# Performance work log

Hardware: AMD Instinct MI355X
Metric: run time of the kernel (lower is better)

The kernel has to match this reference:

```python
import jax, jax.numpy as jnp
import numpy as np

S, B, IN, HID, H, D, DFF, L, NC, EMB = 1024, 32, 3072, 256, 16, 16, 1024, 4, 1623, 10


def setup_inputs() -> dict:
    key = jax.random.key(0)
    ks = jax.random.split(key, 12)
    w = lambda k, shp: 0.02 * jax.random.normal(k, shp, dtype=jnp.float32)
    return {
        "x": jax.random.normal(ks[0], (S, B, IN), dtype=jnp.float32),
        "fb": jax.random.randint(ks[1], (S, B), 0, NC),
        "fc1_w": w(ks[2], (HID, IN)),
        "fc1_b": jnp.zeros((HID,), jnp.float32),
        "emb": w(ks[3], (NC, EMB)),
        "proj_w": w(ks[4], (HID, HID + EMB)),
        "proj_b": jnp.zeros((HID,), jnp.float32),
        "ln1_g": jnp.ones((L, HID), jnp.float32),
        "ln1_b": jnp.zeros((L, HID), jnp.float32),
        "slow_w": w(ks[5], (L, H * (3 * D + 1), HID)),
        "out_w": w(ks[6], (L, HID, H * D)),
        "ln2_g": jnp.ones((L, HID), jnp.float32),
        "ln2_b": jnp.zeros((L, HID), jnp.float32),
        "ff1_w": w(ks[7], (L, DFF, HID)),
        "ff1_b": jnp.zeros((L, DFF), jnp.float32),
        "ff2_w": w(ks[8], (L, HID, DFF)),
        "ff2_b": jnp.zeros((L, HID), jnp.float32),
        "outl_w": w(ks[9], (NC, HID)),
        "outl_b": jnp.zeros((NC,), jnp.float32),
    }


def _ln(x, g, b):
    m = jnp.mean(x, -1, keepdims=True)
    v = jnp.mean(jnp.square(x - m), -1, keepdims=True)
    return (x - m) * jax.lax.rsqrt(v + 1e-5) * g + b


def _delta_attn(x, g, b, sw, ow):
    # x: (S, B, HID); delta-rule fast-weight linear attention
    s, bsz, _ = x.shape
    qkvb = jnp.einsum('sbi,oi->sbo', _ln(x, g, b), sw).reshape(s, bsz, H, 3 * D + 1)
    q, k, v, beta = jnp.split(qkvb, [D, 2 * D, 3 * D], axis=-1)
    q = jax.nn.softmax(q, axis=-1)      # sum-normalized feature map
    k = jax.nn.softmax(k, axis=-1)
    beta = jax.nn.sigmoid(beta)         # (S,B,H,1)

    def step(W, inp):
        qt, kt, vt, bt = inp            # (B,H,D),(B,H,D),(B,H,D),(B,H,1)
        v_old = jnp.einsum('bhkv,bhk->bhv', W, kt)
        v_new = bt * vt + (1.0 - bt) * v_old
        W = W + jnp.einsum('bhk,bhv->bhkv', kt, v_new - v_old)
        return W, jnp.einsum('bhkv,bhk->bhv', W, qt)

    W0 = jnp.zeros((bsz, H, D, D), x.dtype)
    _, o = jax.lax.scan(step, W0, (q, k, v, beta))   # o: (S,B,H,D)
    return x + jnp.einsum('sbi,oi->sbo', o.reshape(s, bsz, H * D), ow)


def _ffn(x, g, b, w1, b1, w2, b2):
    h = jax.nn.relu(jnp.einsum('sbi,oi->sbo', _ln(x, g, b), w1) + b1)
    return x + jnp.einsum('sbi,oi->sbo', h, w2) + b2


def reference(x, fb, fc1_w, fc1_b, emb, proj_w, proj_b, ln1_g, ln1_b, slow_w,
              out_w, ln2_g, ln2_b, ff1_w, ff1_b, ff2_w, ff2_b, outl_w, outl_b):
    h = jnp.einsum('sbi,oi->sbo', x, fc1_w) + fc1_b
    h = jnp.concatenate([h, emb[fb]], axis=-1)
    h = jnp.einsum('sbi,oi->sbo', h, proj_w) + proj_b
    for l in range(L):
        h = _delta_attn(h, ln1_g[l], ln1_b[l], slow_w[l], out_w[l])
        h = _ffn(h, ln2_g[l], ln2_b[l], ff1_w[l], ff1_b[l], ff2_w[l], ff2_b[l])
    return jnp.einsum('sbi,oi->sbo', h, outl_w) + outl_b
```

## Files before the change

### kernel.cpp

```cpp
#include <hip/hip_runtime.h>
#include <hip/hip_bf16.h>

#define S_LEN  1024
#define B_SZ   32
#define IN_DIM 3072
#define HID    256
#define NHEAD  16
#define HDIM   16
#define DFF    1024
#define NLAYER 4
#define NCLS   1623
#define EMB_D  10
#define MROWS  (S_LEN * B_SZ)
#define QROW   56

using bf16   = __hip_bfloat16;
using short8 = __attribute__((ext_vector_type(8))) short;
using f32x4  = __attribute__((ext_vector_type(4))) float;

#define GLOAD16(g, l) __builtin_amdgcn_global_load_lds(                        \
    (const __attribute__((address_space(1))) void*)(g),                        \
    (__attribute__((address_space(3))) void*)(l), 16, 0, 0)

__device__ __forceinline__ float b2f(short s) {
    union { float f; unsigned u; } x;
    x.u = ((unsigned)(unsigned short)s) << 16;
    return x.f;
}

template<int FLAGS>
__global__ __launch_bounds__(256) void mgemm(
    const bf16* __restrict__ A, const bf16* __restrict__ W,
    const float* __restrict__ bias, void* C, int N, int K, int Wld)
{
    __shared__ bf16 sA[2][128 * 32];
    __shared__ bf16 sB[2][128 * 32];
    const int t    = threadIdx.x;
    const int lane = t & 63;
    const int wid  = t >> 6;
    const int wr   = wid >> 1, wc = wid & 1;
    const long bm  = (long)blockIdx.x * 128;
    const int  bn  = blockIdx.y * 128;
    const int  fr  = lane & 15;
    const int  fg  = lane >> 4;
    const int  row0 = t >> 2;
    const int  kq0  = (t & 3) << 3;

    f32x4 acc[4][4];
#pragma unroll
    for (int m = 0; m < 4; ++m)
#pragma unroll
        for (int n = 0; n < 4; ++n)
#pragma unroll
            for (int r = 0; r < 4; ++r) acc[m][n][r] = 0.f;

    const int nkt = K >> 5;

    auto stage = [&](int buf, int kt) {
        const int k0 = kt << 5;
        GLOAD16(A + (bm + row0)      * (long)K   + k0 + kq0, &sA[buf][(t      ) * 8]);
        GLOAD16(A + (bm + row0 + 64) * (long)K   + k0 + kq0, &sA[buf][(t + 256) * 8]);
        GLOAD16(W + (long)(bn + row0)      * Wld + k0 + kq0, &sB[buf][(t      ) * 8]);
        GLOAD16(W + (long)(bn + row0 + 64) * Wld + k0 + kq0, &sB[buf][(t + 256) * 8]);
    };

    stage(0, 0);
    __syncthreads();
    for (int kt = 0; kt < nkt; ++kt) {
        const int cur = kt & 1;
        if (kt + 1 < nkt) stage(cur ^ 1, kt + 1);
        short8 af[4], bg[4];
#pragma unroll
        for (int m = 0; m < 4; ++m)
            af[m] = *(const short8*)&sA[cur][(wr * 64 + m * 16 + fr) * 32 + fg * 8];
#pragma unroll
        for (int n = 0; n < 4; ++n)
            bg[n] = *(const short8*)&sB[cur][(wc * 64 + n * 16 + fr) * 32 + fg * 8];
#pragma unroll
        for (int m = 0; m < 4; ++m)
#pragma unroll
            for (int n = 0; n < 4; ++n)
                acc[m][n] = __builtin_amdgcn_mfma_f32_16x16x32_bf16(
                    af[m], bg[n], acc[m][n], 0, 0, 0);
        __syncthreads();
    }

    float bs[4];
#pragma unroll
    for (int n = 0; n < 4; ++n) {
        const int c = bn + wc * 64 + n * 16 + fr;
        bs[n] = ((FLAGS & 1) && c < N) ? bias[c] : 0.f;
    }
#pragma unroll
    for (int m = 0; m < 4; ++m) {
#pragma unroll
        for (int n = 0; n < 4; ++n) {
            const int c = bn + wc * 64 + n * 16 + fr;
            if (c < N) {
#pragma unroll
                for (int r = 0; r < 4; ++r) {
                    const long rw = bm + wr * 64 + m * 16 + fg * 4 + r;
                    float v = acc[m][n][r] + bs[n];
                    if (FLAGS & 2) v = fmaxf(v, 0.f);
                    if (FLAGS & 16) {
                        const int s = (int)(rw >> 5), b = (int)(rw & 31);
                        const int hh = c / 49, cc = c - hh * 49;
                        if (cc == 48) v = 1.f / (1.f + __expf(-v));
                        ((bf16*)C)[((long)(b * 16 + hh) * 1024 + s) * QROW + cc] =
                            __float2bfloat16(v);
                    } else if (FLAGS & 8) {
                        ((bf16*)C)[rw * N + c] = __float2bfloat16(v);
                    } else {
                        ((float*)C)[rw * N + c] = v;
                    }
                }
            }
        }
    }
}

template<int FLAGS>
__global__ __launch_bounds__(256) void gemm_ln(
    const bf16* __restrict__ A, const bf16* __restrict__ W,
    const float* __restrict__ bias, const float* __restrict__ lg,
    const float* __restrict__ lb, float* H, bf16* __restrict__ Y, int K)
{
    __shared__ bf16 sA[2][64 * 32];
    __shared__ bf16 sB[2][256 * 32];
    __shared__ float rsum[64][4];
    __shared__ float rsq[64][4];
    const int t    = threadIdx.x;
    const int lane = t & 63;
    const int w    = t >> 6;
    const int fr   = lane & 15;
    const int fg   = lane >> 4;
    const long bm  = (long)blockIdx.x * 64;

    f32x4 acc[4][4];
#pragma unroll
    for (int m = 0; m < 4; ++m)
#pragma unroll
        for (int n = 0; n < 4; ++n)
#pragma unroll
            for (int r = 0; r < 4; ++r) acc[m][n][r] = 0.f;

    const int nkt = K >> 5;
    auto stage = [&](int buf, int kt) {
        const int k0 = kt << 5;
        GLOAD16(A + (bm + (t >> 2)) * (long)K + k0 + ((t & 3) << 3),
                &sA[buf][t * 8]);
#pragma unroll
        for (int i = 0; i < 4; ++i)
            GLOAD16(W + (long)((i << 6) + (t >> 2)) * K + k0 + ((t & 3) << 3),
                    &sB[buf][(i * 256 + t) * 8]);
    };

    stage(0, 0);
    __syncthreads();
    for (int kt = 0; kt < nkt; ++kt) {
        const int cur = kt & 1;
        if (kt + 1 < nkt) stage(cur ^ 1, kt + 1);
        short8 af[4], bg[4];
#pragma unroll
        for (int m = 0; m < 4; ++m)
            af[m] = *(const short8*)&sA[cur][(m * 16 + fr) * 32 + fg * 8];
#pragma unroll
        for (int n = 0; n < 4; ++n)
            bg[n] = *(const short8*)&sB[cur][(w * 64 + n * 16 + fr) * 32 + fg * 8];
#pragma unroll
        for (int m = 0; m < 4; ++m)
#pragma unroll
            for (int n = 0; n < 4; ++n)
                acc[m][n] = __builtin_amdgcn_mfma_f32_16x16x32_bf16(
                    af[m], bg[n], acc[m][n], 0, 0, 0);
        __syncthreads();
    }

    float bs[4];
#pragma unroll
    for (int n = 0; n < 4; ++n) {
        const int c = w * 64 + n * 16 + fr;
        bs[n] = (FLAGS & 1) ? bias[c] : 0.f;
    }
    float ps[4][4], pq[4][4];
#pragma unroll
    for (int m = 0; m < 4; ++m)
#pragma unroll
        for (int r = 0; r < 4; ++r) { ps[m][r] = 0.f; pq[m][r] = 0.f; }
#pragma unroll
    for (int m = 0; m < 4; ++m)
#pragma unroll
        for (int n = 0; n < 4; ++n)
#pragma unroll
            for (int r = 0; r < 4; ++r) {
                const long rw = bm + m * 16 + fg * 4 + r;
                const int c = w * 64 + n * 16 + fr;
                float v = acc[m][n][r] + bs[n];
                if (FLAGS & 4) v += H[rw * HID + c];
                H[rw * HID + c] = v;
                acc[m][n][r] = v;
                ps[m][r] += v;
                pq[m][r] += v * v;
            }
    if (FLAGS & 8) {
#pragma unroll
        for (int m = 0; m < 4; ++m)
#pragma unroll
            for (int n = 0; n < 4; ++n)
#pragma unroll
                for (int r = 0; r < 4; ++r) {
                    const long rw = bm + m * 16 + fg * 4 + r;
                    const int c = w * 64 + n * 16 + fr;
                    Y[rw * HID + c] = __float2bfloat16(acc[m][n][r]);
                }
    } else {
#pragma unroll
        for (int m = 0; m < 4; ++m)
#pragma unroll
            for (int r = 0; r < 4; ++r) {
                float s = ps[m][r], q = pq[m][r];
                s += __shfl_xor(s, 1); q += __shfl_xor(q, 1);
                s += __shfl_xor(s, 2); q += __shfl_xor(q, 2);
                s += __shfl_xor(s, 4); q += __shfl_xor(q, 4);
                s += __shfl_xor(s, 8); q += __shfl_xor(q, 8);
                ps[m][r] = s; pq[m][r] = q;
            }
        if (fr == 0) {
#pragma unroll
            for (int m = 0; m < 4; ++m)
#pragma unroll
                for (int r = 0; r < 4; ++r) {
                    const int row = m * 16 + fg * 4 + r;
                    rsum[row][w] = ps[m][r];
                    rsq[row][w]  = pq[m][r];
                }
        }
        __syncthreads();
#pragma unroll
        for (int m = 0; m < 4; ++m)
#pragma unroll
            for (int r = 0; r < 4; ++r) {
                const int row = m * 16 + fg * 4 + r;
                const float4 s4 = *(const float4*)&rsum[row][0];
                const float4 q4 = *(const float4*)&rsq[row][0];
                const float S = (s4.x + s4.y) + (s4.z + s4.w);
                const float Q = (q4.x + q4.y) + (q4.z + q4.w);
                const float mean = S * (1.f / 256.f);
                const float inv  = rsqrtf(Q * (1.f / 256.f) - mean * mean + 1e-5f);
                const long rw = bm + row;
#pragma unroll
                for (int n = 0; n < 4; ++n) {
                    const int c = w * 64 + n * 16 + fr;
                    const float y = (acc[m][n][r] - mean) * inv * lg[c] + lb[c];
                    Y[rw * HID + c] = __float2bfloat16(y);
                }
            }
    }
}

__global__ __launch_bounds__(256) void fc1_k(
    const float* __restrict__ A, const bf16* __restrict__ W,
    const float* __restrict__ bias, bf16* __restrict__ hcat)
{
    __shared__ bf16 sA[2][128 * 32];
    __shared__ bf16 sB[2][128 * 32];
    const int t    = threadIdx.x;
    const int lane = t & 63;
    const int wid  = t >> 6;
    const int wr   = wid >> 1, wc = wid & 1;
    const long bm  = (long)blockIdx.x * 128;
    const int  bn  = blockIdx.y * 128;
    const int  fr  = lane & 15;
    const int  fg  = lane >> 4;
    const int  row0 = t >> 2;
    const int  kq0  = (t & 3) << 3;
    const int  arow = t >> 3;
    const int  ac4  = (t & 7) << 2;

    f32x4 acc[4][4];
#pragma unroll
    for (int m = 0; m < 4; ++m)
#pragma unroll
        for (int n = 0; n < 4; ++n)
#pragma unroll
            for (int r = 0; r < 4; ++r) acc[m][n][r] = 0.f;

    auto stageB = [&](int buf, int kt) {
        const int k0 = kt << 5;
        GLOAD16(W + (long)(bn + row0)      * IN_DIM + k0 + kq0, &sB[buf][(t      ) * 8]);
        GLOAD16(W + (long)(bn + row0 + 64) * IN_DIM + k0 + kq0, &sB[buf][(t + 256) * 8]);
    };
    float4 va[4];
    auto loadA = [&](int kt) {
        const int k0 = kt << 5;
#pragma unroll
        for (int rep = 0; rep < 4; ++rep)
            va[rep] = *(const float4*)(A + (bm + arow + rep * 32) * (long)IN_DIM + k0 + ac4);
    };
    auto writeA = [&](int buf) {
#pragma unroll
        for (int rep = 0; rep < 4; ++rep) {
            alignas(8) bf16 tb[4];
            tb[0] = __float2bfloat16(va[rep].x);
            tb[1] = __float2bfloat16(va[rep].y);
            tb[2] = __float2bfloat16(va[rep].z);
            tb[3] = __float2bfloat16(va[rep].w);
            *(ushort4*)&sA[buf][(arow + rep * 32) * 32 + ac4] = *(const ushort4*)tb;
        }
    };

    loadA(0);
    stageB(0, 0);
    writeA(0);
    __syncthreads();
    const int nkt = IN_DIM >> 5;
    for (int kt = 0; kt < nkt; ++kt) {
        const int cur = kt & 1;
        if (kt + 1 < nkt) { stageB(cur ^ 1, kt + 1); loadA(kt + 1); }
        short8 af[4], bg[4];
#pragma unroll
        for (int m = 0; m < 4; ++m)
            af[m] = *(const short8*)&sA[cur][(wr * 64 + m * 16 + fr) * 32 + fg * 8];
#pragma unroll
        for (int n = 0; n < 4; ++n)
            bg[n] = *(const short8*)&sB[cur][(wc * 64 + n * 16 + fr) * 32 + fg * 8];
#pragma unroll
        for (int m = 0; m < 4; ++m)
#pragma unroll
            for (int n = 0; n < 4; ++n)
                acc[m][n] = __builtin_amdgcn_mfma_f32_16x16x32_bf16(
                    af[m], bg[n], acc[m][n], 0, 0, 0);
        if (kt + 1 < nkt) writeA(cur ^ 1);
        __syncthreads();
    }

#pragma unroll
    for (int n = 0; n < 4; ++n) {
        const int c = bn + wc * 64 + n * 16 + fr;
        const float bsn = bias[c];
#pragma unroll
        for (int m = 0; m < 4; ++m)
#pragma unroll
            for (int r = 0; r < 4; ++r) {
                const long rw = bm + wr * 64 + m * 16 + fg * 4 + r;
                hcat[rw * 288 + c] = __float2bfloat16(acc[m][n][r] + bsn);
            }
    }
}

__global__ __launch_bounds__(256) void fillemb(
    const float* __restrict__ emb, const int* __restrict__ fb,
    bf16* __restrict__ hcat)
{
    const long row = (long)blockIdx.x * 8 + (threadIdx.x >> 5);
    const int c = threadIdx.x & 31;
    bf16 v = (c < EMB_D) ? __float2bfloat16(emb[(long)fb[row] * EMB_D + c])
                         : __float2bfloat16(0.f);
    hcat[row * 288 + 256 + c] = v;
}

__global__ __launch_bounds__(256) void cvtall(
    const float* __restrict__ fc1_w, const float* __restrict__ proj_w,
    const float* __restrict__ slow_w, const float* __restrict__ out_w,
    const float* __restrict__ ff1_w, const float* __restrict__ ff2_w,
    const float* __restrict__ outl_w, bf16* __restrict__ dst)
{
    for (long i = (long)blockIdx.x * 256 + threadIdx.x; i < 4562944L;
         i += (long)gridDim.x * 256) {
        float v;
        if (i < 786432L) {
            v = fc1_w[i];
        } else if (i < 860160L) {
            const long j = i - 786432L;
            const int r = (int)(j / 288), c = (int)(j - (long)r * 288);
            v = (c < 266) ? proj_w[(long)r * 266 + c] : 0.f;
        } else if (i < 1777664L) {
            const long j = i - 860160L;
            const int l = (int)(j / 229376);
            const long m = j - (long)l * 229376;
            const int r = (int)(m >> 8), c = (int)(m & 255);
            v = (r < 784) ? slow_w[(long)l * 200704 + (long)r * 256 + c] : 0.f;
        } else if (i < 2039808L) {
            v = out_w[i - 1777664L];
        } else if (i < 3088384L) {
            v = ff1_w[i - 2039808L];
        } else if (i < 4136960L) {
            v = ff2_w[i - 3088384L];
        } else {
            const long j = i - 4136960L;
            const int r = (int)(j >> 8), c = (int)(j & 255);
            v = (r < 1623) ? outl_w[(long)r * 256 + c] : 0.f;
        }
        dst[i] = __float2bfloat16(v);
    }
}

#define DOT16(dst, kr, s0, s1, s2, s3) do {                                    \
    float _pa = fmaf(kr[3],  (s0).w, fmaf(kr[2],  (s0).z, fmaf(kr[1],  (s0).y, kr[0]  * (s0).x))); \
    float _pb = fmaf(kr[7],  (s1).w, fmaf(kr[6],  (s1).z, fmaf(kr[5],  (s1).y, kr[4]  * (s1).x))); \
    float _pc = fmaf(kr[11], (s2).w, fmaf(kr[10], (s2).z, fmaf(kr[9],  (s2).y, kr[8]  * (s2).x))); \
    float _pd = fmaf(kr[15], (s3).w, fmaf(kr[14], (s3).z, fmaf(kr[13], (s3).y, kr[12] * (s3).x))); \
    dst = (_pa + _pb) + (_pc + _pd);                                           \
} while (0)

__global__ __launch_bounds__(256) void coef_k(
    const bf16* __restrict__ qkvb, float* __restrict__ cfb)
{
    __shared__ float wrkc[4][16 * 52];
    __shared__ float Gm[4][16 * 17];
    __shared__ float Mql[4][16 * 17];
    const int tid = threadIdx.x;
    const int w = tid >> 6, lane = tid & 63;
    const int cg = blockIdx.x * 4 + w;
    const int chain = cg >> 6;
    const int ck = cg & 63;
    const bf16* rows = qkvb + ((long)chain * S_LEN + (long)ck * 16) * QROW;
    float* wk = wrkc[w];
    float* G  = Gm[w];
    float* M  = Mql[w];

    if (lane < 32) {
        const int row = lane >> 1, hf = lane & 1;
        const short* ps = (const short*)(rows + (long)row * QROW) + hf * 16;
        const short8 r0 = *(const short8*)(ps);
        const short8 r1 = *(const short8*)(ps + 8);
        float f[16];
#pragma unroll
        for (int j = 0; j < 8; ++j) { f[j] = b2f(r0[j]); f[8 + j] = b2f(r1[j]); }
        float mx = f[0];
#pragma unroll
        for (int j = 1; j < 16; ++j) mx = fmaxf(mx, f[j]);
        float sum = 0.f;
#pragma unroll
        for (int j = 0; j < 16; ++j) { f[j] = __expf(f[j] - mx); sum += f[j]; }
        const float inv = 1.f / sum;
        float* pw = wk + row * 52 + hf * 16;
#pragma unroll
        for (int j = 0; j < 16; ++j) pw[j] = f[j] * inv;
        if (hf == 0)
            wk[row * 52 + 48] = b2f(((const short*)(rows + (long)row * QROW))[48]);
    }
    asm volatile("s_waitcnt lgkmcnt(0)" ::: "memory");

    const int i4 = lane >> 2, jq = lane & 3;
    {
        const float* myrow = wk + i4 * 52;
        float ki[16], qi[16];
        const float4 kA = *(const float4*)(myrow + 16);
        const float4 kB = *(const float4*)(myrow + 20);
        const float4 kC = *(const float4*)(myrow + 24);
        const float4 kD = *(const float4*)(myrow + 28);
        ki[0]=kA.x; ki[1]=kA.y; ki[2]=kA.z; ki[3]=kA.w;
        ki[4]=kB.x; ki[5]=kB.y; ki[6]=kB.z; ki[7]=kB.w;
        ki[8]=kC.x; ki[9]=kC.y; ki[10]=kC.z; ki[11]=kC.w;
        ki[12]=kD.x; ki[13]=kD.y; ki[14]=kD.z; ki[15]=kD.w;
        const float4 qA = *(const float4*)(myrow);
        const float4 qB = *(const float4*)(myrow + 4);
        const float4 qC = *(const float4*)(myrow + 8);
        const float4 qD = *(const float4*)(myrow + 12);
        qi[0]=qA.x; qi[1]=qA.y; qi[2]=qA.z; qi[3]=qA.w;
        qi[4]=qB.x; qi[5]=qB.y; qi[6]=qB.z; qi[7]=qB.w;
        qi[8]=qC.x; qi[9]=qC.y; qi[10]=qC.z; qi[11]=qC.w;
        qi[12]=qD.x; qi[13]=qD.y; qi[14]=qD.z; qi[15]=qD.w;
        const float beta = myrow[48];
#pragma unroll
        for (int m = 0; m < 4; ++m) {
            const int s = jq * 4 + m;
            const float* sr = wk + s * 52 + 16;
            const float4 s0 = *(const float4*)(sr);
            const float4 s1 = *(const float4*)(sr + 4);
            const float4 s2 = *(const float4*)(sr + 8);
            const float4 s3 = *(const float4*)(sr + 12);
            float g, qk;
            DOT16(g, ki, s0, s1, s2, s3);
            DOT16(qk, qi, s0, s1, s2, s3);
            G[i4 * 17 + s] = (s < i4)  ? beta * g : 0.f;
            M[i4 * 17 + s] = (s <= i4) ? qk : 0.f;
        }
    }
    asm volatile("s_waitcnt lgkmcnt(0)" ::: "memory");

    {
        const int cs = i4, rq = jq;
        float A1r[4], A2r[4];
#pragma unroll
        for (int j = 0; j < 4; ++j)
            A1r[j] = M[(rq * 4 + j) * 17 + cs];
        const float4 kcol = *(const float4*)&wk[cs * 52 + 16 + rq * 4];
        A2r[0] = kcol.x; A2r[1] = kcol.y; A2r[2] = kcol.z; A2r[3] = kcol.w;
#pragma unroll
        for (int t = 15; t >= 1; --t) {
            const float Lc = G[t * 17 + cs];
            const float b10 = __shfl(A1r[0], t * 4 + rq);
            const float b11 = __shfl(A1r[1], t * 4 + rq);
            const float b12 = __shfl(A1r[2], t * 4 + rq);
            const float b13 = __shfl(A1r[3], t * 4 + rq);
            const float b20 = __shfl(A2r[0], t * 4 + rq);
            const float b21 = __shfl(A2r[1], t * 4 + rq);
            const float b22 = __shfl(A2r[2], t * 4 + rq);
            const float b23 = __shfl(A2r[3], t * 4 + rq);
            A1r[0] = fmaf(-Lc, b10, A1r[0]); A1r[1] = fmaf(-Lc, b11, A1r[1]);
            A1r[2] = fmaf(-Lc, b12, A1r[2]); A1r[3] = fmaf(-Lc, b13, A1r[3]);
            A2r[0] = fmaf(-Lc, b20, A2r[0]); A2r[1] = fmaf(-Lc, b21, A2r[1]);
            A2r[2] = fmaf(-Lc, b22, A2r[2]); A2r[3] = fmaf(-Lc, b23, A2r[3]);
        }
        float* dst = cfb + (long)cg * 512;
        f32x4 o1; o1[0]=A1r[0]; o1[1]=A1r[1]; o1[2]=A1r[2]; o1[3]=A1r[3];
        f32x4 o2; o2[0]=A2r[0]; o2[1]=A2r[1]; o2[2]=A2r[2]; o2[3]=A2r[3];
        *(f32x4*)(dst + cs * 16 + rq * 4) = o1;
        *(f32x4*)(dst + 256 + cs * 16 + rq * 4) = o2;
    }
}

__global__ __launch_bounds__(64) void scan11(
    const bf16* __restrict__ qkvb, const float* __restrict__ cfb,
    bf16* __restrict__ o)
{
    __shared__ short sbf[2][2048];
    __shared__ float scf[2][1024];
    __shared__ float wrk[32 * 52];
    __shared__ float W0l[16 * 20];
    __shared__ float EVl[16 * 20];
    const int lane = threadIdx.x;
    const int i4 = lane >> 2;
    const int jq = lane & 3;
    const int chain = blockIdx.x;
    const int b = chain >> 4, hh = chain & 15;
    const char* cbb = (const char*)(qkvb + (long)chain * S_LEN * QROW);
    bf16* po = o + (long)b * HID + hh * HDIM + jq * 4;

    for (int z = lane; z < 320; z += 64) W0l[z] = 0.f;

    auto stage = [&](int buf, int nb2) {
#pragma unroll
        for (int iss = 0; iss < 4; ++iss) {
            const char* src = cbb + (long)nb2 * 3584 + (iss * 64 + lane) * 16;
            GLOAD16(src, &sbf[buf][(iss * 64 + lane) * 8]);
        }
        const float* csrc = cfb + ((long)chain * 64 + nb2 * 2) * 512;
#pragma unroll
        for (int iss = 0; iss < 4; ++iss)
            GLOAD16(csrc + (iss * 64 + lane) * 4, &scf[buf][(iss * 64 + lane) * 4]);
    };

    stage(0, 0);
    asm volatile("s_waitcnt vmcnt(0)" ::: "memory");
    for (int nb = 0; nb < 32; ++nb) {
        const int buf = nb & 1;
        asm volatile("s_waitcnt vmcnt(2)" ::: "memory");
        if (nb + 1 < 32) stage(buf ^ 1, nb + 1);

        {
            const int row = lane >> 1, hf = lane & 1;
            const short* ps = &sbf[buf][row * QROW + hf * 16];
            const short8 r0 = *(const short8*)(ps);
            const short8 r1 = *(const short8*)(ps + 8);
            float f[16];
#pragma unroll
            for (int j = 0; j < 8; ++j) { f[j] = b2f(r0[j]); f[8 + j] = b2f(r1[j]); }
            float mx = f[0];
#pragma unroll
            for (int j = 1; j < 16; ++j) mx = fmaxf(mx, f[j]);
            float sum = 0.f;
#pragma unroll
            for (int j = 0; j < 16; ++j) { f[j] = __expf(f[j] - mx); sum += f[j]; }
            const float inv = 1.f / sum;
            float* pw = wrk + row * 52 + hf * 16;
#pragma unroll
            for (int j = 0; j < 16; ++j) pw[j] = f[j] * inv;
            const short8 rv = *(const short8*)(&sbf[buf][row * QROW + 32 + hf * 8]);
            float* pv = wrk + row * 52 + 32 + hf * 8;
#pragma unroll
            for (int j = 0; j < 8; ++j) pv[j] = b2f(rv[j]);
            if (hf == 0)
                wrk[row * 52 + 48] = b2f(sbf[buf][row * QROW + 48]);
        }
        asm volatile("s_waitcnt lgkmcnt(0)" ::: "memory");

#pragma unroll
        for (int t = 0; t < 2; ++t) {
            const float* rb = wrk + t * 16 * 52;
            const float* myrow = rb + i4 * 52;
            float QKTr[16], KT2r[16];
#pragma unroll
            for (int s = 0; s < 16; ++s) {
                QKTr[s] = scf[buf][t * 512 + s * 16 + i4];
                KT2r[s] = scf[buf][t * 512 + 256 + s * 16 + i4];
            }
            float ki[16], qi[16];
            {
                const float4 kA = *(const float4*)(myrow + 16);
                const float4 kB = *(const float4*)(myrow + 20);
                const float4 kC = *(const float4*)(myrow + 24);
                const float4 kD = *(const float4*)(myrow + 28);
                ki[0]=kA.x; ki[1]=kA.y; ki[2]=kA.z; ki[3]=kA.w;
                ki[4]=kB.x; ki[5]=kB.y; ki[6]=kB.z; ki[7]=kB.w;
                ki[8]=kC.x; ki[9]=kC.y; ki[10]=kC.z; ki[11]=kC.w;
                ki[12]=kD.x; ki[13]=kD.y; ki[14]=kD.z; ki[15]=kD.w;
                const float4 qA = *(const float4*)(myrow);
                const float4 qB = *(const float4*)(myrow + 4);
                const float4 qC = *(const float4*)(myrow + 8);
                const float4 qD = *(const float4*)(myrow + 12);
                qi[0]=qA.x; qi[1]=qA.y; qi[2]=qA.z; qi[3]=qA.w;
                qi[4]=qB.x; qi[5]=qB.y; qi[6]=qB.z; qi[7]=qB.w;
                qi[8]=qC.x; qi[9]=qC.y; qi[10]=qC.z; qi[11]=qC.w;
                qi[12]=qD.x; qi[13]=qD.y; qi[14]=qD.z; qi[15]=qD.w;
            }
            const float beta = myrow[48];
            float P0=0,P1=0,P2=0,P3=0, O0=0,O1=0,O2=0,O3=0;
#pragma unroll
            for (int x = 0; x < 16; ++x) {
                const float4 w = *(const float4*)&W0l[x * 20 + jq * 4];
                P0 = fmaf(ki[x], w.x, P0); P1 = fmaf(ki[x], w.y, P1);
                P2 = fmaf(ki[x], w.z, P2); P3 = fmaf(ki[x], w.w, P3);
                O0 = fmaf(qi[x], w.x, O0); O1 = fmaf(qi[x], w.y, O1);
                O2 = fmaf(qi[x], w.z, O2); O3 = fmaf(qi[x], w.w, O3);
            }
            const float4 vv = *(const float4*)(myrow + 32 + jq * 4);
            f32x4 ev;
            ev[0] = beta * (vv.x - P0); ev[1] = beta * (vv.y - P1);
            ev[2] = beta * (vv.z - P2); ev[3] = beta * (vv.w - P3);
            *(f32x4*)&EVl[i4 * 20 + jq * 4] = ev;
            asm volatile("s_waitcnt lgkmcnt(0)" ::: "memory");
            float a0=0,a1=0,a2=0,a3=0;
#pragma unroll
            for (int s = 0; s < 16; ++s) {
                const float4 es = *(const float4*)&EVl[s * 20 + jq * 4];
                O0 = fmaf(QKTr[s], es.x, O0); O1 = fmaf(QKTr[s], es.y, O1);
                O2 = fmaf(QKTr[s], es.z, O2); O3 = fmaf(QKTr[s], es.w, O3);
                a0 = fmaf(KT2r[s], es.x, a0); a1 = fmaf(KT2r[s], es.y, a1);
                a2 = fmaf(KT2r[s], es.z, a2); a3 = fmaf(KT2r[s], es.w, a3);
            }
            {
                const int sg = nb * 32 + t * 16 + i4;
                alignas(8) bf16 tb[4];
                tb[0] = __float2bfloat16(O0); tb[1] = __float2bfloat16(O1);
                tb[2] = __float2bfloat16(O2); tb[3] = __float2bfloat16(O3);
                *(ushort4*)((unsigned short*)(po + (long)sg * (B_SZ * HID))) =
                    *(const ushort4*)tb;
            }
            {
                float4 w = *(const float4*)&W0l[i4 * 20 + jq * 4];
                w.x += a0; w.y += a1; w.z += a2; w.w += a3;
                *(float4*)&W0l[i4 * 20 + jq * 4] = w;
            }
            asm volatile("s_waitcnt lgkmcnt(0)" ::: "memory");
        }
    }
}

extern "C" void kernel_launch(void* const* d_in, const int* in_sizes, int n_in,
                              void* d_out, int out_size, void* d_ws, size_t ws_size,
                              hipStream_t stream)
{
    const float* x      = (const float*)d_in[0];
    const int*   fb     = (const int*)  d_in[1];
    const float* fc1_w  = (const float*)d_in[2];
    const float* fc1_b  = (const float*)d_in[3];
    const float* emb    = (const float*)d_in[4];
    const float* proj_w = (const float*)d_in[5];
    const float* proj_b = (const float*)d_in[6];
    const float* ln1_g  = (const float*)d_in[7];
    const float* ln1_b  = (const float*)d_in[8];
    const float* slow_w = (const float*)d_in[9];
    const float* out_w  = (const float*)d_in[10];
    const float* ln2_g  = (const float*)d_in[11];
    const float* ln2_b  = (const float*)d_in[12];
    const float* ff1_w  = (const float*)d_in[13];
    const float* ff1_b  = (const float*)d_in[14];
    const float* ff2_w  = (const float*)d_in[15];
    const float* ff2_b  = (const float*)d_in[16];
    const float* outl_w = (const float*)d_in[17];
    const float* outl_b = (const float*)d_in[18];

    char* wp = (char*)d_ws;
    float* h    = (float*)wp;                 wp += (size_t)MROWS * HID * 4;
    bf16*  abuf = (bf16*)wp;                  wp += (size_t)MROWS * HID * 2;
    bf16*  fc1b = (bf16*)wp;                  wp += (size_t)HID * IN_DIM * 2;
    bf16*  projb= (bf16*)wp;                  wp += (size_t)HID * 288 * 2;
    bf16*  slowb= (bf16*)wp;                  wp += (size_t)NLAYER * 896 * HID * 2;
    bf16*  outwb= (bf16*)wp;                  wp += (size_t)NLAYER * HID * HID * 2;
    bf16*  ff1b = (bf16*)wp;                  wp += (size_t)NLAYER * DFF * HID * 2;
    bf16*  ff2b = (bf16*)wp;                  wp += (size_t)NLAYER * HID * DFF * 2;
    bf16*  outlb= (bf16*)wp;                  wp += (size_t)1664 * HID * 2;

    bf16*  hcat = (bf16*)d_out;
    bf16*  qkvb = (bf16*)d_out;
    float* cfb  = (float*)((bf16*)d_out + (size_t)512 * 1024 * QROW);
    bf16*  hff  = (bf16*)d_out;

    const dim3 blk(256);

    cvtall<<<dim3(1024), blk, 0, stream>>>(fc1_w, proj_w, slow_w, out_w,
                                           ff1_w, ff2_w, outl_w, fc1b);

    fc1_k<<<dim3(256, 2), blk, 0, stream>>>(x, fc1b, fc1_b, hcat);
    fillemb<<<dim3(MROWS / 8), blk, 0, stream>>>(emb, fb, hcat);
    gemm_ln<1><<<dim3(512), blk, 0, stream>>>(hcat, projb, proj_b,
                                              ln1_g, ln1_b, h, abuf, 288);

    for (int l = 0; l < NLAYER; ++l) {
        mgemm<16><<<dim3(256, 7), blk, 0, stream>>>(abuf, slowb + (size_t)l * 896 * HID,
                                                    nullptr, qkvb, 784, HID, HID);
        coef_k<<<dim3(8192), blk, 0, stream>>>(qkvb, cfb);
        scan11<<<dim3(B_SZ * NHEAD), dim3(64), 0, stream>>>(qkvb, cfb, abuf);
        gemm_ln<4><<<dim3(512), blk, 0, stream>>>(abuf, outwb + (size_t)l * HID * HID,
                                                  nullptr, ln2_g + l * HID,
                                                  ln2_b + l * HID, h, abuf, HID);
        mgemm<11><<<dim3(256, 8), blk, 0, stream>>>(abuf, ff1b + (size_t)l * DFF * HID,
                                                    ff1_b + l * DFF, hff, DFF, HID, HID);
        if (l + 1 < NLAYER)
            gemm_ln<5><<<dim3(512), blk, 0, stream>>>(hff, ff2b + (size_t)l * HID * DFF,
                                                      ff2_b + l * HID,
                                                      ln1_g + (l + 1) * HID,
                                                      ln1_b + (l + 1) * HID, h, abuf, DFF);
        else
            gemm_ln<13><<<dim3(512), blk, 0, stream>>>(hff, ff2b + (size_t)l * HID * DFF,
                                                       ff2_b + l * HID,
                                                       nullptr, nullptr, h, abuf, DFF);
    }
    mgemm<1><<<dim3(256, 13), blk, 0, stream>>>(abuf, outlb, outl_b, d_out,
                                                NCLS, HID, HID);
}
```

Baseline: 1.571 ms.

## Precompute per-chunk affine transition matrices so the sequential scan is a matrix prefix

The coefficient kernel now builds, for each 16-step chunk, the full affine transition (M, C, N, D matrices) that maps the incoming fast-weight state to the outgoing state and the chunk outputs. The sequential scan kernel then only applies these 16x16 matrices chunk by chunk, using register shuffles, with no softmax, loads of q/k/v, or intra-chunk solve on the critical serial path. This moves parallelizable work out of the 512-block serial scan into the highly parallel coefficient kernel. The cost is twice the coefficient buffer traffic (1024 floats per chunk) and more work in coef2_k.

```diff
diff --git a/kernel.cpp b/kernel.cpp
--- a/kernel.cpp
+++ b/kernel.cpp
@@ -403,12 +403,14 @@
     dst = (_pa + _pb) + (_pc + _pd);                                           \
 } while (0)
 
-__global__ __launch_bounds__(256) void coef_k(
+__global__ __launch_bounds__(256) void coef2_k(
     const bf16* __restrict__ qkvb, float* __restrict__ cfb)
 {
     __shared__ float wrkc[4][16 * 52];
     __shared__ float Gm[4][16 * 17];
     __shared__ float Mql[4][16 * 17];
+    __shared__ float A1l[4][16 * 17];
+    __shared__ float A2l[4][16 * 17];
     const int tid = threadIdx.x;
     const int w = tid >> 6, lane = tid & 63;
     const int cg = blockIdx.x * 4 + w;
@@ -418,6 +420,8 @@
     float* wk = wrkc[w];
     float* G  = Gm[w];
     float* M  = Mql[w];
+    float* A1 = A1l[w];
+    float* A2 = A2l[w];
 
     if (lane < 32) {
         const int row = lane >> 1, hf = lane & 1;
@@ -437,6 +441,10 @@
         float* pw = wk + row * 52 + hf * 16;
 #pragma unroll
         for (int j = 0; j < 16; ++j) pw[j] = f[j] * inv;
+        const short8 rv = *(const short8*)((const short*)(rows + (long)row * QROW) + 32 + hf * 8);
+        float* pv = wk + row * 52 + 32 + hf * 8;
+#pragma unroll
+        for (int j = 0; j < 8; ++j) pv[j] = b2f(rv[j]);
         if (hf == 0)
             wk[row * 52 + 48] = b2f(((const short*)(rows + (long)row * QROW))[48]);
     }
@@ -504,148 +512,105 @@
             A2r[0] = fmaf(-Lc, b20, A2r[0]); A2r[1] = fmaf(-Lc, b21, A2r[1]);
             A2r[2] = fmaf(-Lc, b22, A2r[2]); A2r[3] = fmaf(-Lc, b23, A2r[3]);
         }
-        float* dst = cfb + (long)cg * 512;
-        f32x4 o1; o1[0]=A1r[0]; o1[1]=A1r[1]; o1[2]=A1r[2]; o1[3]=A1r[3];
-        f32x4 o2; o2[0]=A2r[0]; o2[1]=A2r[1]; o2[2]=A2r[2]; o2[3]=A2r[3];
-        *(f32x4*)(dst + cs * 16 + rq * 4) = o1;
-        *(f32x4*)(dst + 256 + cs * 16 + rq * 4) = o2;
-    }
-}
-
-__global__ __launch_bounds__(64) void scan11(
-    const bf16* __restrict__ qkvb, const float* __restrict__ cfb,
-    bf16* __restrict__ o)
-{
-    __shared__ short sbf[2][2048];
+        const float bcs = wk[cs * 52 + 48];
+#pragma unroll
+        for (int j = 0; j < 4; ++j) {
+            A1[(rq * 4 + j) * 17 + cs] = A1r[j] * bcs;
+            A2[(rq * 4 + j) * 17 + cs] = A2r[j] * bcs;
+        }
+    }
+    asm volatile("s_waitcnt lgkmcnt(0)" ::: "memory");
+
+    {
+        const int x = i4;
+        float mM[4] = {0,0,0,0}, mN[4] = {0,0,0,0};
+        float mC[4] = {0,0,0,0}, mD[4] = {0,0,0,0};
+#pragma unroll
+        for (int s = 0; s < 16; ++s) {
+            const float a2 = A2[x * 17 + s];
+            const float a1 = A1[x * 17 + s];
+            const float4 k4 = *(const float4*)&wk[s * 52 + 16 + jq * 4];
+            const float4 v4 = *(const float4*)&wk[s * 52 + 32 + jq * 4];
+            mM[0] = fmaf(a2, k4.x, mM[0]); mM[1] = fmaf(a2, k4.y, mM[1]);
+            mM[2] = fmaf(a2, k4.z, mM[2]); mM[3] = fmaf(a2, k4.w, mM[3]);
+            mN[0] = fmaf(a2, v4.x, mN[0]); mN[1] = fmaf(a2, v4.y, mN[1]);
+            mN[2] = fmaf(a2, v4.z, mN[2]); mN[3] = fmaf(a2, v4.w, mN[3]);
+            mC[0] = fmaf(a1, k4.x, mC[0]); mC[1] = fmaf(a1, k4.y, mC[1]);
+            mC[2] = fmaf(a1, k4.z, mC[2]); mC[3] = fmaf(a1, k4.w, mC[3]);
+            mD[0] = fmaf(a1, v4.x, mD[0]); mD[1] = fmaf(a1, v4.y, mD[1]);
+            mD[2] = fmaf(a1, v4.z, mD[2]); mD[3] = fmaf(a1, v4.w, mD[3]);
+        }
+        const float4 qx = *(const float4*)&wk[x * 52 + jq * 4];
+        float* dst = cfb + (long)cg * 1024;
+        f32x4 oM, oC, oN, oD;
+#pragma unroll
+        for (int m = 0; m < 4; ++m)
+            oM[m] = ((jq * 4 + m) == x ? 1.f : 0.f) - mM[m];
+        oC[0] = qx.x - mC[0]; oC[1] = qx.y - mC[1];
+        oC[2] = qx.z - mC[2]; oC[3] = qx.w - mC[3];
+        oN[0] = mN[0]; oN[1] = mN[1]; oN[2] = mN[2]; oN[3] = mN[3];
+        oD[0] = mD[0]; oD[1] = mD[1]; oD[2] = mD[2]; oD[3] = mD[3];
+        *(f32x4*)(dst +       x * 16 + jq * 4) = oM;
+        *(f32x4*)(dst + 256 + x * 16 + jq * 4) = oC;
+        *(f32x4*)(dst + 512 + x * 16 + jq * 4) = oN;
+        *(f32x4*)(dst + 768 + x * 16 + jq * 4) = oD;
+    }
+}
+
+__global__ __launch_bounds__(64) void prefix_k(
+    const float* __restrict__ cfb, bf16* __restrict__ o)
+{
     __shared__ float scf[2][1024];
-    __shared__ float wrk[32 * 52];
-    __shared__ float W0l[16 * 20];
-    __shared__ float EVl[16 * 20];
     const int lane = threadIdx.x;
-    const int i4 = lane >> 2;
-    const int jq = lane & 3;
+    const int x = lane >> 2, jq = lane & 3;
     const int chain = blockIdx.x;
     const int b = chain >> 4, hh = chain & 15;
-    const char* cbb = (const char*)(qkvb + (long)chain * S_LEN * QROW);
     bf16* po = o + (long)b * HID + hh * HDIM + jq * 4;
-
-    for (int z = lane; z < 320; z += 64) W0l[z] = 0.f;
-
-    auto stage = [&](int buf, int nb2) {
-#pragma unroll
-        for (int iss = 0; iss < 4; ++iss) {
-            const char* src = cbb + (long)nb2 * 3584 + (iss * 64 + lane) * 16;
-            GLOAD16(src, &sbf[buf][(iss * 64 + lane) * 8]);
-        }
-        const float* csrc = cfb + ((long)chain * 64 + nb2 * 2) * 512;
-#pragma unroll
-        for (int iss = 0; iss < 4; ++iss)
-            GLOAD16(csrc + (iss * 64 + lane) * 4, &scf[buf][(iss * 64 + lane) * 4]);
+    const float* cb = cfb + (long)chain * 64 * 1024;
+
+    auto stage = [&](int buf, int c) {
+#pragma unroll
+        for (int i = 0; i < 4; ++i)
+            GLOAD16(cb + (long)c * 1024 + (i * 64 + lane) * 4,
+                    &scf[buf][(i * 64 + lane) * 4]);
     };
 
+    float W0r = 0.f, W1r = 0.f, W2r = 0.f, W3r = 0.f;
     stage(0, 0);
     asm volatile("s_waitcnt vmcnt(0)" ::: "memory");
-    for (int nb = 0; nb < 32; ++nb) {
-        const int buf = nb & 1;
-        asm volatile("s_waitcnt vmcnt(2)" ::: "memory");
-        if (nb + 1 < 32) stage(buf ^ 1, nb + 1);
-
-        {
-            const int row = lane >> 1, hf = lane & 1;
-            const short* ps = &sbf[buf][row * QROW + hf * 16];
-            const short8 r0 = *(const short8*)(ps);
-            const short8 r1 = *(const short8*)(ps + 8);
-            float f[16];
-#pragma unroll
-            for (int j = 0; j < 8; ++j) { f[j] = b2f(r0[j]); f[8 + j] = b2f(r1[j]); }
-            float mx = f[0];
-#pragma unroll
-            for (int j = 1; j < 16; ++j) mx = fmaxf(mx, f[j]);
-            float sum = 0.f;
-#pragma unroll
-            for (int j = 0; j < 16; ++j) { f[j] = __expf(f[j] - mx); sum += f[j]; }
-            const float inv = 1.f / sum;
-            float* pw = wrk + row * 52 + hf * 16;
-#pragma unroll
-            for (int j = 0; j < 16; ++j) pw[j] = f[j] * inv;
-            const short8 rv = *(const short8*)(&sbf[buf][row * QROW + 32 + hf * 8]);
-            float* pv = wrk + row * 52 + 32 + hf * 8;
-#pragma unroll
-            for (int j = 0; j < 8; ++j) pv[j] = b2f(rv[j]);
-            if (hf == 0)
-                wrk[row * 52 + 48] = b2f(sbf[buf][row * QROW + 48]);
-        }
-        asm volatile("s_waitcnt lgkmcnt(0)" ::: "memory");
-
-#pragma unroll
-        for (int t = 0; t < 2; ++t) {
-            const float* rb = wrk + t * 16 * 52;
-            const float* myrow = rb + i4 * 52;
-            float QKTr[16], KT2r[16];
-#pragma unroll
-            for (int s = 0; s < 16; ++s) {
-                QKTr[s] = scf[buf][t * 512 + s * 16 + i4];
-                KT2r[s] = scf[buf][t * 512 + 256 + s * 16 + i4];
-            }
-            float ki[16], qi[16];
-            {
-                const float4 kA = *(const float4*)(myrow + 16);
-                const float4 kB = *(const float4*)(myrow + 20);
-                const float4 kC = *(const float4*)(myrow + 24);
-                const float4 kD = *(const float4*)(myrow + 28);
-                ki[0]=kA.x; ki[1]=kA.y; ki[2]=kA.z; ki[3]=kA.w;
-                ki[4]=kB.x; ki[5]=kB.y; ki[6]=kB.z; ki[7]=kB.w;
-                ki[8]=kC.x; ki[9]=kC.y; ki[10]=kC.z; ki[11]=kC.w;
-                ki[12]=kD.x; ki[13]=kD.y; ki[14]=kD.z; ki[15]=kD.w;
-                const float4 qA = *(const float4*)(myrow);
-                const float4 qB = *(const float4*)(myrow + 4);
-                const float4 qC = *(const float4*)(myrow + 8);
-                const float4 qD = *(const float4*)(myrow + 12);
-                qi[0]=qA.x; qi[1]=qA.y; qi[2]=qA.z; qi[3]=qA.w;
-                qi[4]=qB.x; qi[5]=qB.y; qi[6]=qB.z; qi[7]=qB.w;
-                qi[8]=qC.x; qi[9]=qC.y; qi[10]=qC.z; qi[11]=qC.w;
-                qi[12]=qD.x; qi[13]=qD.y; qi[14]=qD.z; qi[15]=qD.w;
-            }
-            const float beta = myrow[48];
-            float P0=0,P1=0,P2=0,P3=0, O0=0,O1=0,O2=0,O3=0;
-#pragma unroll
-            for (int x = 0; x < 16; ++x) {
-                const float4 w = *(const float4*)&W0l[x * 20 + jq * 4];
-                P0 = fmaf(ki[x], w.x, P0); P1 = fmaf(ki[x], w.y, P1);
-                P2 = fmaf(ki[x], w.z, P2); P3 = fmaf(ki[x], w.w, P3);
-                O0 = fmaf(qi[x], w.x, O0); O1 = fmaf(qi[x], w.y, O1);
-                O2 = fmaf(qi[x], w.z, O2); O3 = fmaf(qi[x], w.w, O3);
-            }
-            const float4 vv = *(const float4*)(myrow + 32 + jq * 4);
-            f32x4 ev;
-            ev[0] = beta * (vv.x - P0); ev[1] = beta * (vv.y - P1);
-            ev[2] = beta * (vv.z - P2); ev[3] = beta * (vv.w - P3);
-            *(f32x4*)&EVl[i4 * 20 + jq * 4] = ev;
-            asm volatile("s_waitcnt lgkmcnt(0)" ::: "memory");
-            float a0=0,a1=0,a2=0,a3=0;
-#pragma unroll
-            for (int s = 0; s < 16; ++s) {
-                const float4 es = *(const float4*)&EVl[s * 20 + jq * 4];
-                O0 = fmaf(QKTr[s], es.x, O0); O1 = fmaf(QKTr[s], es.y, O1);
-                O2 = fmaf(QKTr[s], es.z, O2); O3 = fmaf(QKTr[s], es.w, O3);
-                a0 = fmaf(KT2r[s], es.x, a0); a1 = fmaf(KT2r[s], es.y, a1);
-                a2 = fmaf(KT2r[s], es.z, a2); a3 = fmaf(KT2r[s], es.w, a3);
-            }
-            {
-                const int sg = nb * 32 + t * 16 + i4;
-                alignas(8) bf16 tb[4];
-                tb[0] = __float2bfloat16(O0); tb[1] = __float2bfloat16(O1);
-                tb[2] = __float2bfloat16(O2); tb[3] = __float2bfloat16(O3);
-                *(ushort4*)((unsigned short*)(po + (long)sg * (B_SZ * HID))) =
-                    *(const ushort4*)tb;
-            }
-            {
-                float4 w = *(const float4*)&W0l[i4 * 20 + jq * 4];
-                w.x += a0; w.y += a1; w.z += a2; w.w += a3;
-                *(float4*)&W0l[i4 * 20 + jq * 4] = w;
-            }
-            asm volatile("s_waitcnt lgkmcnt(0)" ::: "memory");
-        }
+    for (int c = 0; c < 64; ++c) {
+        const int buf = c & 1;
+        asm volatile("s_waitcnt vmcnt(1)" ::: "memory");
+        if (c + 1 < 64) stage(buf ^ 1, c + 1);
+
+        float Mrow[16], Crow[16];
+#pragma unroll
+        for (int t = 0; t < 16; ++t) {
+            Mrow[t] = scf[buf][x * 16 + t];
+            Crow[t] = scf[buf][256 + x * 16 + t];
+        }
+        const float4 N4 = *(const float4*)&scf[buf][512 + x * 16 + jq * 4];
+        const float4 D4 = *(const float4*)&scf[buf][768 + x * 16 + jq * 4];
+        float Wn0 = N4.x, Wn1 = N4.y, Wn2 = N4.z, Wn3 = N4.w;
+        float On0 = D4.x, On1 = D4.y, On2 = D4.z, On3 = D4.w;
+#pragma unroll
+        for (int t = 0; t < 16; ++t) {
+            const float g0 = __shfl(W0r, t * 4 + jq);
+            const float g1 = __shfl(W1r, t * 4 + jq);
+            const float g2 = __shfl(W2r, t * 4 + jq);
+            const float g3 = __shfl(W3r, t * 4 + jq);
+            Wn0 = fmaf(Mrow[t], g0, Wn0); Wn1 = fmaf(Mrow[t], g1, Wn1);
+            Wn2 = fmaf(Mrow[t], g2, Wn2); Wn3 = fmaf(Mrow[t], g3, Wn3);
+            On0 = fmaf(Crow[t], g0, On0); On1 = fmaf(Crow[t], g1, On1);
+            On2 = fmaf(Crow[t], g2, On2); On3 = fmaf(Crow[t], g3, On3);
+        }
+        W0r = Wn0; W1r = Wn1; W2r = Wn2; W3r = Wn3;
+        const int sg = c * 16 + x;
+        alignas(8) bf16 tb[4];
+        tb[0] = __float2bfloat16(On0); tb[1] = __float2bfloat16(On1);
+        tb[2] = __float2bfloat16(On2); tb[3] = __float2bfloat16(On3);
+        *(ushort4*)((unsigned short*)(po + (long)sg * (B_SZ * HID))) =
+            *(const ushort4*)tb;
     }
 }
 
@@ -702,8 +667,8 @@
     for (int l = 0; l < NLAYER; ++l) {
         mgemm<16><<<dim3(256, 7), blk, 0, stream>>>(abuf, slowb + (size_t)l * 896 * HID,
                                                     nullptr, qkvb, 784, HID, HID);
-        coef_k<<<dim3(8192), blk, 0, stream>>>(qkvb, cfb);
-        scan11<<<dim3(B_SZ * NHEAD), dim3(64), 0, stream>>>(qkvb, cfb, abuf);
+        coef2_k<<<dim3(8192), blk, 0, stream>>>(qkvb, cfb);
+        prefix_k<<<dim3(B_SZ * NHEAD), dim3(64), 0, stream>>>(cfb, abuf);
         gemm_ln<4><<<dim3(512), blk, 0, stream>>>(abuf, outwb + (size_t)l * HID * HID,
                                                   nullptr, ln2_g + l * HID,
                                                   ln2_b + l * HID, h, abuf, HID);
```

Result: faster. 1.533 ms (-2.5%).
